# Kernel optimization log

Measured on AMD Instinct MI355X. Metric: run time of the kernel, lower is better.

Reference implementation:

```python
import jax, jax.numpy as jnp
import numpy as np
from jax import lax

B, L, D_IN, H, RES, BD, D_OUT = 1024, 128, 5, 64, 256, 8, 1


def setup_inputs() -> dict:
    key = jax.random.key(0)
    ks = jax.random.split(key, 14)
    f = jnp.float32
    d = {}
    d["V_noise"] = jax.random.normal(ks[0], (B, D_IN), f)
    d["increments"] = jax.random.normal(ks[1], (B, L, BD), f)
    d["W1"] = jax.random.normal(ks[2], (H, D_IN), f) / np.float32(np.sqrt(D_IN))
    d["b1"] = jnp.zeros((H,), f)
    d["W2"] = jax.random.normal(ks[3], (RES, H), f) / np.float32(np.sqrt(H))
    d["b2"] = jnp.zeros((RES,), f)
    d["rho1"] = jax.random.normal(ks[4], (1, 1), f)
    d["rho2"] = jax.random.normal(ks[5], (1, 1), f)
    d["rho3"] = jax.random.normal(ks[6], (1, 1), f)
    d["rho4"] = jax.random.normal(ks[7], (1, 1), f)
    d["rho5"] = jax.random.normal(ks[8], (1, 1), f)
    # scale reservoir matrices by 1/sqrt(res) so pre-activations are O(1)
    d["B1"] = jax.random.normal(ks[9], (RES, RES), f) / np.float32(np.sqrt(RES))
    d["B2"] = jax.random.normal(ks[10], (BD, RES, RES), f) / np.float32(np.sqrt(RES))
    d["lambda1"] = jax.random.normal(ks[11], (RES, 1), f)
    d["lambda2"] = jax.random.normal(ks[12], (BD, RES, 1), f)
    d["Wr"] = jax.random.normal(ks[13], (D_OUT, RES), f) / np.float32(np.sqrt(RES))
    d["br"] = jnp.zeros((D_OUT,), f)
    return d


def reference(V_noise, increments, W1, b1, W2, b2,
              rho1, rho2, rho3, rho4, rho5,
              B1, B2, lambda1, lambda2, Wr, br):
    act = jnp.tanh
    # initial-condition MLP: [B, D_in] -> [B, RES]
    V = act(V_noise @ W1.T + b1) @ W2.T + b2
    # Brownian path with W[:,0] = 0
    Wp = jnp.cumsum(increments, axis=1).at[:, 0, :].set(0.0)
    dW = Wp[:, 1:] - Wp[:, :-1]          # [B, L-1, BD]
    l1 = lambda1[:, 0]                    # [RES]
    l2 = lambda2[:, :, 0]                 # [BD, RES]
    rho5s = rho5[0, 0]

    def step(r, dw):                      # r: [B, RES], dw: [B, BD]
        drift = act(rho1 * (r @ B1.T) + rho2 * l1)                      # [B, RES]
        diff = act(rho3 * jnp.einsum('kij,bj->bki', B2, r) + rho4 * l2)  # [B, BD, RES]
        rn = r + drift + rho5s * jnp.einsum('bki,bk->bi', diff, dw)
        return rn, rn

    _, Rs = lax.scan(step, V, jnp.swapaxes(dW, 0, 1))  # [L-1, B, RES]
    Rall = jnp.concatenate([V[None], Rs], axis=0)       # [L, B, RES]
    # time-homogeneous linear readout per lag, concatenated along time
    x = Rall @ Wr.T + br                                 # [L, B, D_out]
    out = jnp.transpose(x, (1, 0, 2)).reshape(V.shape[0], Rall.shape[0] * x.shape[-1], 1)
    return out
```

## Files before the change

### kernel.cpp

```cpp
#include <hip/hip_runtime.h>
#include <hip/hip_bf16.h>

#define B_TOT 1024
#define L_T   128
#define DIN   5
#define HD    64
#define RESN  256
#define BDN   8
#define NMAT  9
#define NROWS (NMAT * RESN)
#define PLANE ((size_t)NROWS * RESN)
#define NGRP  16
#define BG    64
#define FPB   16
#define NTHR  256
#define RB_GRP_BYTES (2 * 16 * 2 * BG * FPB * 2)
#define GRP_SHORTS (RB_GRP_BYTES / 2)
#define BUF_SHORTS 32768
#define WS_RB_OFF  (2 * PLANE * 2)
#define WS_FLAG_OFF (WS_RB_OFF + (size_t)NGRP * RB_GRP_BYTES)
#define FLAGS_PER_GRP 1024

typedef __attribute__((ext_vector_type(8))) short bf16x8;
typedef __attribute__((ext_vector_type(4))) float f32x4;
typedef __attribute__((ext_vector_type(4))) unsigned u32x4;

__device__ __forceinline__ float fast_tanh(float x) {
    float e = __expf(2.0f * x);
    return 1.0f - 2.0f * __builtin_amdgcn_rcpf(e + 1.0f);
}

__device__ __forceinline__ void split_hl(float v, unsigned short& h, unsigned short& l) {
    __hip_bfloat16 hb = __float2bfloat16(v);
    h = __builtin_bit_cast(unsigned short, hb);
    l = __builtin_bit_cast(unsigned short, __float2bfloat16(v - __bfloat162float(hb)));
}

__device__ __forceinline__ unsigned mall_load1(const unsigned* p) {
    unsigned r;
    asm volatile("global_load_dword %0, %1, off sc0 sc1" : "=v"(r) : "v"(p));
    return r;
}
__device__ __forceinline__ unsigned l2_load1(const unsigned* p) {
    unsigned r;
    asm volatile("global_load_dword %0, %1, off sc0" : "=v"(r) : "v"(p));
    return r;
}
__device__ __forceinline__ void mall_store1(unsigned* p, unsigned v) {
    asm volatile("global_store_dword %0, %1, off sc0 sc1" :: "v"(p), "v"(v) : "memory");
}
__device__ __forceinline__ void l2_store1(unsigned* p, unsigned v) {
    asm volatile("global_store_dword %0, %1, off" :: "v"(p), "v"(v) : "memory");
}
__device__ __forceinline__ u32x4 mall_load4s(const unsigned short* p) {
    u32x4 r;
    asm volatile("global_load_dwordx4 %0, %1, off sc0 sc1" : "=v"(r) : "v"(p));
    return r;
}
__device__ __forceinline__ u32x4 l2_load4s(const unsigned short* p) {
    u32x4 r;
    asm volatile("global_load_dwordx4 %0, %1, off sc0" : "=v"(r) : "v"(p));
    return r;
}
__device__ __forceinline__ void mall_store4(unsigned short* p, u32x4 v) {
    asm volatile("global_store_dwordx4 %0, %1, off sc0 sc1" :: "v"(p), "v"(v) : "memory");
}
__device__ __forceinline__ void l2_store4(unsigned short* p, u32x4 v) {
    asm volatile("global_store_dwordx4 %0, %1, off" :: "v"(p), "v"(v) : "memory");
}
__device__ __forceinline__ void atom_addf_l2(float* p, float v) {
    asm volatile("global_atomic_add_f32 %0, %1, off" :: "v"(p), "v"(v) : "memory");
}
__device__ __forceinline__ void wait_vm0() {
    asm volatile("s_waitcnt vmcnt(0)" ::: "memory");
}
__device__ __forceinline__ void wait_lgkm0() {
    asm volatile("s_waitcnt lgkmcnt(0)" ::: "memory");
}

__device__ __forceinline__ void spin_all(const unsigned* fladdr, unsigned want, bool l2m) {
    unsigned guard = 0;
    for (;;) {
        unsigned fv = l2m ? l2_load1(fladdr) : mall_load1(fladdr);
        wait_vm0();
        if (__ballot(fv < want) == 0ull) break;
        __builtin_amdgcn_s_sleep(1);
        if (++guard > (1u << 20)) break;
    }
}

__global__ void conv_w(const float* __restrict__ B1, const float* __restrict__ B2,
                       __hip_bfloat16* __restrict__ wh, __hip_bfloat16* __restrict__ wl) {
    int idx = blockIdx.x * 256 + threadIdx.x;
    float v = (idx < RESN * RESN) ? B1[idx] : B2[idx - RESN * RESN];
    __hip_bfloat16 h = __float2bfloat16(v);
    wh[idx] = h;
    wl[idx] = __float2bfloat16(v - __bfloat162float(h));
}

__global__ __launch_bounds__(NTHR, 1) void sde_ws(
    const float* __restrict__ Vn,  const float* __restrict__ inc,
    const float* __restrict__ W1,  const float* __restrict__ b1,
    const float* __restrict__ W2,  const float* __restrict__ b2,
    const float* __restrict__ rho1p, const float* __restrict__ rho2p,
    const float* __restrict__ rho3p, const float* __restrict__ rho4p,
    const float* __restrict__ rho5p,
    const float* __restrict__ lam1, const float* __restrict__ lam2,
    const float* __restrict__ Wr,  const float* __restrict__ brp,
    const __hip_bfloat16* __restrict__ wbf,
    unsigned short* __restrict__ rbs,
    unsigned int* __restrict__ flags,
    float* __restrict__ out)
{
    __shared__ __align__(16) short wlds[2][NMAT][8][64][8];
    __shared__ __align__(16) unsigned short stage[4][512];
    __shared__ int l2mode_sh;

    const int tid  = threadIdx.x;
    const int mt   = tid >> 6;
    const int lane = tid & 63;
    const int n16  = lane & 15;
    const int quad = lane >> 4;
    const int bx   = blockIdx.x;
    const int g    = ((bx & 7) << 1) | (bx >> 7);
    const int fb   = (bx >> 3) & 15;
    const int f0   = fb * FPB;
    const int b0g  = g * BG;
    unsigned short* gbs = rbs + (size_t)g * GRP_SHORTS;
    unsigned int* flagp  = flags + g * FLAGS_PER_GRP;
    unsigned int* myflag = flagp + (fb * 4 + mt) * 16;
    const unsigned* fladdr = (const unsigned*)(flagp + ((lane & 15) * 4 + mt) * 16);
    unsigned* regtbl = flags + NGRP * FLAGS_PER_GRP;
    unsigned* regcnt = regtbl + 256;

    if (tid == 0) {
        unsigned xcd;
        asm volatile("s_getreg_b32 %0, hwreg(HW_REG_XCC_ID)" : "=s"(xcd));
        mall_store1(&regtbl[bx], xcd);
        wait_vm0();
        __hip_atomic_fetch_add(regcnt, 1u, __ATOMIC_RELAXED, __HIP_MEMORY_SCOPE_AGENT);
    }

    const float rho1 = rho1p[0], rho2 = rho2p[0], rho3 = rho3p[0],
                rho4 = rho4p[0], rho5 = rho5p[0];
    const float brv = brp[0];
    const float bradd = (fb == 0) ? brv : 0.0f;

    float* hf  = (float*)&wlds[0][0][0][0][0];
    float* vsh = hf + 64 * 66;
    for (int p = tid; p < BG * HD; p += NTHR) {
        int b = p >> 6, hh = p & 63;
        float s = b1[hh];
        #pragma unroll
        for (int d = 0; d < DIN; ++d) s += Vn[(b0g + b) * DIN + d] * W1[hh * DIN + d];
        hf[b * 66 + hh] = fast_tanh(s);
    }
    __syncthreads();

    if (tid == 0) {
        unsigned cnt, guard = 0;
        do {
            cnt = mall_load1(regcnt);
            wait_vm0();
            if (cnt >= 256) break;
            __builtin_amdgcn_s_sleep(1);
        } while (++guard < (1u << 22));
        unsigned e[16];
        #pragma unroll
        for (int q = 0; q < 16; ++q)
            e[q] = mall_load1(&regtbl[((g & 1) << 7) | (q << 3) | (g >> 1)]);
        wait_vm0();
        int ok = (cnt >= 256) ? 1 : 0;
        #pragma unroll
        for (int q = 1; q < 16; ++q) ok &= (e[q] == e[0]) ? 1 : 0;
        l2mode_sh = ok;
    }
    __syncthreads();
    const bool l2m = (l2mode_sh != 0);

    {
        int bl = lane >> 2;
        int b  = 16 * mt + bl;
        #pragma unroll
        for (int i = 0; i < 4; ++i) {
            int f = (lane & 3) * 4 + i;
            float s = b2[f0 + f];
            #pragma unroll 8
            for (int hh = 0; hh < HD; ++hh) s += hf[b * 66 + hh] * W2[(f0 + f) * HD + hh];
            vsh[b * 16 + f] = s;
            unsigned short h_, l_;
            split_hl(s, h_, l_);
            stage[mt][0 * 256 + bl * 16 + f] = h_;
            stage[mt][1 * 256 + bl * 16 + f] = l_;
        }
        wait_lgkm0();
        u32x4 v = *(const u32x4*)&stage[mt][lane * 8];
        unsigned short* dst = gbs + 0 * BUF_SHORTS + fb * 2048 +
                              (lane >> 5) * 1024 + 16 * mt * 16 + (lane & 31) * 8;
        if (l2m) l2_store4(dst, v); else mall_store4(dst, v);
    }
    wait_vm0();
    if (lane == 0) {
        if (l2m) l2_store1(myflag, 1u);
        else __hip_atomic_fetch_add(myflag, 1u, __ATOMIC_RELAXED, __HIP_MEMORY_SCOPE_AGENT);
    }

    float rmast[4];
    #pragma unroll
    for (int rg = 0; rg < 4; ++rg) rmast[rg] = vsh[(16 * mt + 4 * quad + rg) * 16 + n16];
    const float l1c = lam1[f0 + n16];
    const float wrv = Wr[f0 + n16];
    float l2c[BDN];
    #pragma unroll
    for (int k = 0; k < BDN; ++k) l2c[k] = lam2[k * RESN + f0 + n16];
    __syncthreads();

    for (int e = tid; e < 2 * NMAT * 8 * 64; e += NTHR) {
        int l  = e & 63;
        int kk = (e >> 6) & 7;
        int m  = e >> 9;
        int pl = (m >= NMAT) ? 1 : 0;
        int nt = m - pl * NMAT;
        const uint4* src = (const uint4*)(wbf + (size_t)pl * PLANE +
            (size_t)(nt * RESN + f0 + (l & 15)) * RESN + kk * 32 + (l >> 4) * 8);
        *(uint4*)&wlds[pl][nt][kk][l][0] = *src;
    }
    __syncthreads();

    const unsigned short* pcb = gbs + (quad >> 1) * 2048 + (16 * mt + n16) * 16 + (quad & 1) * 8;

    for (int t = 0; t < L_T; ++t) {
        {
            float po[4];
            #pragma unroll
            for (int rg = 0; rg < 4; ++rg) {
                float p = wrv * rmast[rg];
                p += __shfl_xor(p, 1);
                p += __shfl_xor(p, 2);
                p += __shfl_xor(p, 4);
                p += __shfl_xor(p, 8);
                po[rg] = p;
            }
            if (n16 == 0) {
                #pragma unroll
                for (int rg = 0; rg < 4; ++rg) {
                    float* op = out + (size_t)(b0g + 16 * mt + 4 * quad + rg) * L_T + t;
                    float v = po[rg] + bradd;
                    if (l2m) atom_addf_l2(op, v);
                    else __hip_atomic_fetch_add(op, v, __ATOMIC_RELAXED, __HIP_MEMORY_SCOPE_AGENT);
                }
            }
        }
        if (t == L_T - 1) break;

        float dwv[4][8];
        #pragma unroll
        for (int rg = 0; rg < 4; ++rg) {
            const size_t bglob = (size_t)(b0g + 16 * mt + 4 * quad + rg) * (L_T * BDN);
            const float4 d0 = *(const float4*)(inc + bglob + (size_t)(t + 1) * BDN);
            const float4 d1 = *(const float4*)(inc + bglob + (size_t)(t + 1) * BDN + 4);
            dwv[rg][0] = d0.x; dwv[rg][1] = d0.y; dwv[rg][2] = d0.z; dwv[rg][3] = d0.w;
            dwv[rg][4] = d1.x; dwv[rg][5] = d1.y; dwv[rg][6] = d1.z; dwv[rg][7] = d1.w;
            if (t == 0) {
                const float4 e0 = *(const float4*)(inc + bglob);
                const float4 e1 = *(const float4*)(inc + bglob + 4);
                dwv[rg][0] += e0.x; dwv[rg][1] += e0.y; dwv[rg][2] += e0.z; dwv[rg][3] += e0.w;
                dwv[rg][4] += e1.x; dwv[rg][5] += e1.y; dwv[rg][6] += e1.z; dwv[rg][7] += e1.w;
            }
        }
        spin_all(fladdr, (unsigned)(t + 1), l2m);
        const int cur = t & 1, nxt = cur ^ 1;

        bf16x8 afh[8], afl[8];
        {
            const unsigned short* pc = pcb + cur * BUF_SHORTS;
            if (l2m) {
                #pragma unroll
                for (int kk = 0; kk < 8; ++kk) {
                    afh[kk] = __builtin_bit_cast(bf16x8, l2_load4s(pc + kk * 4096));
                    afl[kk] = __builtin_bit_cast(bf16x8, l2_load4s(pc + kk * 4096 + 1024));
                }
            } else {
                #pragma unroll
                for (int kk = 0; kk < 8; ++kk) {
                    afh[kk] = __builtin_bit_cast(bf16x8, mall_load4s(pc + kk * 4096));
                    afl[kk] = __builtin_bit_cast(bf16x8, mall_load4s(pc + kk * 4096 + 1024));
                }
            }
        }
        wait_vm0();

        f32x4 acc[NMAT] = {};
        #pragma unroll
        for (int kk = 0; kk < 8; ++kk) {
            bf16x8 bh[NMAT], bl[NMAT];
            #pragma unroll
            for (int nt = 0; nt < NMAT; ++nt) {
                bh[nt] = *(const bf16x8*)&wlds[0][nt][kk][lane][0];
                bl[nt] = *(const bf16x8*)&wlds[1][nt][kk][lane][0];
            }
            #pragma unroll
            for (int nt = 0; nt < NMAT; ++nt)
                acc[nt] = __builtin_amdgcn_mfma_f32_16x16x32_bf16(afh[kk], bh[nt], acc[nt], 0, 0, 0);
            #pragma unroll
            for (int nt = 0; nt < NMAT; ++nt)
                acc[nt] = __builtin_amdgcn_mfma_f32_16x16x32_bf16(afl[kk], bh[nt], acc[nt], 0, 0, 0);
            #pragma unroll
            for (int nt = 0; nt < NMAT; ++nt)
                acc[nt] = __builtin_amdgcn_mfma_f32_16x16x32_bf16(afh[kk], bl[nt], acc[nt], 0, 0, 0);
        }

        #pragma unroll
        for (int rg = 0; rg < 4; ++rg) {
            float drift = fast_tanh(rho1 * acc[0][rg] + rho2 * l1c);
            float s = 0.0f;
            #pragma unroll
            for (int k = 0; k < BDN; ++k)
                s += fast_tanh(rho3 * acc[1 + k][rg] + rho4 * l2c[k]) * dwv[rg][k];
            float rn = rmast[rg] + drift + rho5 * s;
            rmast[rg] = rn;
            unsigned short h_, l_;
            split_hl(rn, h_, l_);
            stage[mt][0 * 256 + (4 * quad + rg) * 16 + n16] = h_;
            stage[mt][1 * 256 + (4 * quad + rg) * 16 + n16] = l_;
        }
        wait_lgkm0();
        {
            u32x4 v = *(const u32x4*)&stage[mt][lane * 8];
            unsigned short* dst = gbs + nxt * BUF_SHORTS + fb * 2048 +
                                  (lane >> 5) * 1024 + 16 * mt * 16 + (lane & 31) * 8;
            if (l2m) l2_store4(dst, v); else mall_store4(dst, v);
        }
        wait_vm0();
        if (lane == 0) {
            if (l2m) l2_store1(myflag, (unsigned)(t + 2));
            else __hip_atomic_fetch_add(myflag, 1u, __ATOMIC_RELAXED, __HIP_MEMORY_SCOPE_AGENT);
        }
    }
}

extern "C" void kernel_launch(void* const* d_in, const int* in_sizes, int n_in,
                              void* d_out, int out_size, void* d_ws, size_t ws_size,
                              hipStream_t stream) {
    const float* Vn   = (const float*)d_in[0];
    const float* inc  = (const float*)d_in[1];
    const float* W1   = (const float*)d_in[2];
    const float* b1   = (const float*)d_in[3];
    const float* W2   = (const float*)d_in[4];
    const float* b2   = (const float*)d_in[5];
    const float* r1   = (const float*)d_in[6];
    const float* r2   = (const float*)d_in[7];
    const float* r3   = (const float*)d_in[8];
    const float* r4   = (const float*)d_in[9];
    const float* r5   = (const float*)d_in[10];
    const float* B1   = (const float*)d_in[11];
    const float* B2   = (const float*)d_in[12];
    const float* lam1 = (const float*)d_in[13];
    const float* lam2 = (const float*)d_in[14];
    const float* Wr   = (const float*)d_in[15];
    const float* br   = (const float*)d_in[16];

    __hip_bfloat16* wh    = (__hip_bfloat16*)d_ws;
    unsigned short* rbs   = (unsigned short*)((char*)d_ws + WS_RB_OFF);
    unsigned int*   flags = (unsigned int*)((char*)d_ws + WS_FLAG_OFF);
    float* out = (float*)d_out;

    hipMemsetAsync(d_out, 0, out_size, stream);
    hipMemsetAsync(flags, 0, NGRP * FLAGS_PER_GRP * sizeof(unsigned int) + 2048, stream);
    conv_w<<<dim3(NROWS * RESN / 256), dim3(256), 0, stream>>>(B1, B2, wh, wh + PLANE);
    sde_ws<<<dim3(256), dim3(NTHR), 0, stream>>>(
        Vn, inc, W1, b1, W2, b2, r1, r2, r3, r4, r5, lam1, lam2, Wr, br,
        wh, rbs, flags, out);
}
```

Baseline: 772.4 us.

## Assign batch groups by XCD rank so each group's blocks share one L2

Each block now reads its XCD id, takes a rank among the blocks on that XCD with an atomic counter, and block 0 decides whether all eight XCDs hold exactly 32 blocks. If so, the group and feature-block indices come from that XCD-local rank. This guarantees every batch group sits on one XCD, so the L2-mode exchange path is used. Before, L2 mode depended on the hardware placement happening to match a fixed blockIdx mapping. The cost is an extra grid-wide wait on a decision flag before work starts, and the counters in the workspace must be reset between launches.

```diff
diff --git a/kernel.cpp b/kernel.cpp
--- a/kernel.cpp
+++ b/kernel.cpp
@@ -115,6 +115,7 @@
     __shared__ __align__(16) short wlds[2][NMAT][8][64][8];
     __shared__ __align__(16) unsigned short stage[4][512];
     __shared__ int l2mode_sh;
+    __shared__ unsigned rank_sh, xcd_sh;
 
     const int tid  = threadIdx.x;
     const int mt   = tid >> 6;
@@ -122,24 +123,60 @@
     const int n16  = lane & 15;
     const int quad = lane >> 4;
     const int bx   = blockIdx.x;
-    const int g    = ((bx & 7) << 1) | (bx >> 7);
-    const int fb   = (bx >> 3) & 15;
+
+    unsigned* xbase  = flags + NGRP * FLAGS_PER_GRP;
+    unsigned* xcdcnt = xbase;
+    unsigned* totalp = xbase + 8;
+    unsigned* decp   = xbase + 9;
+
+    if (tid == 0) {
+        unsigned xcd;
+        asm volatile("s_getreg_b32 %0, hwreg(HW_REG_XCC_ID)" : "=s"(xcd));
+        xcd &= 7u;
+        unsigned r = __hip_atomic_fetch_add(&xcdcnt[xcd], 1u, __ATOMIC_RELAXED,
+                                            __HIP_MEMORY_SCOPE_AGENT);
+        rank_sh = r;
+        xcd_sh  = xcd;
+        __hip_atomic_fetch_add(totalp, 1u, __ATOMIC_RELAXED, __HIP_MEMORY_SCOPE_AGENT);
+        if (bx == 0) {
+            unsigned cnt = 0, guard = 0;
+            do {
+                cnt = mall_load1(totalp);
+                wait_vm0();
+                if (cnt >= 256u) break;
+                __builtin_amdgcn_s_sleep(8);
+            } while (++guard < (1u << 22));
+            int bal = (cnt >= 256u) ? 1 : 0;
+            unsigned c[8];
+            #pragma unroll
+            for (int q = 0; q < 8; ++q) c[q] = mall_load1(&xcdcnt[q]);
+            wait_vm0();
+            #pragma unroll
+            for (int q = 0; q < 8; ++q) bal &= (c[q] == 32u) ? 1 : 0;
+            mall_store1(decp, 1u + (unsigned)bal);
+            wait_vm0();
+            l2mode_sh = bal;
+        } else {
+            unsigned d = 0, guard = 0;
+            do {
+                d = mall_load1(decp);
+                wait_vm0();
+                if (d != 0u) break;
+                __builtin_amdgcn_s_sleep(8);
+            } while (++guard < (1u << 22));
+            l2mode_sh = (d == 2u) ? 1 : 0;
+        }
+    }
+    __syncthreads();
+    const bool l2m = (l2mode_sh != 0);
+    const int g  = l2m ? (int)(xcd_sh * 2u + (rank_sh >> 4)) : (((bx & 7) << 1) | (bx >> 7));
+    const int fb = l2m ? (int)(rank_sh & 15u) : ((bx >> 3) & 15);
     const int f0   = fb * FPB;
     const int b0g  = g * BG;
     unsigned short* gbs = rbs + (size_t)g * GRP_SHORTS;
     unsigned int* flagp  = flags + g * FLAGS_PER_GRP;
     unsigned int* myflag = flagp + (fb * 4 + mt) * 16;
     const unsigned* fladdr = (const unsigned*)(flagp + ((lane & 15) * 4 + mt) * 16);
-    unsigned* regtbl = flags + NGRP * FLAGS_PER_GRP;
-    unsigned* regcnt = regtbl + 256;
-
-    if (tid == 0) {
-        unsigned xcd;
-        asm volatile("s_getreg_b32 %0, hwreg(HW_REG_XCC_ID)" : "=s"(xcd));
-        mall_store1(&regtbl[bx], xcd);
-        wait_vm0();
-        __hip_atomic_fetch_add(regcnt, 1u, __ATOMIC_RELAXED, __HIP_MEMORY_SCOPE_AGENT);
-    }
 
     const float rho1 = rho1p[0], rho2 = rho2p[0], rho3 = rho3p[0],
                 rho4 = rho4p[0], rho5 = rho5p[0];
@@ -156,27 +193,6 @@
         hf[b * 66 + hh] = fast_tanh(s);
     }
     __syncthreads();
-
-    if (tid == 0) {
-        unsigned cnt, guard = 0;
-        do {
-            cnt = mall_load1(regcnt);
-            wait_vm0();
-            if (cnt >= 256) break;
-            __builtin_amdgcn_s_sleep(1);
-        } while (++guard < (1u << 22));
-        unsigned e[16];
-        #pragma unroll
-        for (int q = 0; q < 16; ++q)
-            e[q] = mall_load1(&regtbl[((g & 1) << 7) | (q << 3) | (g >> 1)]);
-        wait_vm0();
-        int ok = (cnt >= 256) ? 1 : 0;
-        #pragma unroll
-        for (int q = 1; q < 16; ++q) ok &= (e[q] == e[0]) ? 1 : 0;
-        l2mode_sh = ok;
-    }
-    __syncthreads();
-    const bool l2m = (l2mode_sh != 0);
 
     {
         int bl = lane >> 2;
```

Result: no change. 771.2 us (-0.2%).
